# Optimization experiments

Measured on AMD Instinct MI355X. Metric: run time of the kernel, lower is better.

## Reference

```python
import jax, jax.numpy as jnp
import numpy as np

jax.config.update("jax_enable_x64", True)  # original uses complex128 FFTs

H0 = W0 = 3072   # full frame (shp_0)
HC = WC = 2048   # center_dims
MS_H = MS_W = 10
EPS = 1e-8


def setup_inputs() -> dict:
    key = jax.random.key(0)
    k1, k2 = jax.random.split(key)
    # smooth base image so the NCC peak neighborhood is positive (log-valid),
    # as the algorithm assumes for real microscopy data
    base = jax.image.resize(jax.random.normal(k1, (192, 192), jnp.float32), (H0, W0), method="linear")
    fr = jnp.roll(base, (3, -2), axis=(0, 1))[None, :, :, None] + 0.02 * jax.random.normal(k2, (1, H0, W0, 1), jnp.float32)
    template = base[:, :, None, None]
    return {"fr": fr.astype(jnp.float32), "template": template.astype(jnp.float32)}


def _avg_pool_valid(x, kh, kw):
    # x: (1,H,W,C); stride-1 VALID average pool via summed-area table (kernel is huge: ~2028x2028)
    s = jnp.cumsum(jnp.cumsum(x.astype(jnp.float64), axis=1), axis=2)
    s = jnp.pad(s, ((0, 0), (1, 0), (1, 0), (0, 0)))
    H, W = x.shape[1], x.shape[2]
    oh, ow = H - kh + 1, W - kw + 1
    sums = (s[:, kh:kh + oh, kw:kw + ow] - s[:, :oh, kw:kw + ow]
            - s[:, kh:kh + oh, :ow] + s[:, :oh, :ow])
    return (sums / (kh * kw)).astype(x.dtype)


def _extract_fractional_peak(ncc, ms_h, ms_w):
    n = ncc[0, :, :, 0]                     # (2*ms_w+1, 2*ms_h+1)
    W = n.shape[1]
    am = jnp.argmax(n.reshape(-1))
    sx = (am // W).astype(jnp.int32)
    sy = (am % W).astype(jnp.int32)
    log_n = jnp.log(n)
    lxm1 = log_n[sx - 1, sy]
    lxp1 = log_n[sx + 1, sy]
    lym1 = log_n[sx, sy - 1]
    lyp1 = log_n[sx, sy + 1]
    four = 4.0 * log_n[sx, sy]
    sh_x = -(sx - ms_h).astype(jnp.float32) - (lxm1 - lxp1) / (2.0 * lxm1 - four + 2.0 * lxp1)
    sh_y = -(sy - ms_w).astype(jnp.float32) - (lym1 - lyp1) / (2.0 * lym1 - four + 2.0 * lyp1)
    return sh_x.reshape(1, 1), sh_y.reshape(1, 1)


def _translate_bilinear(img, dx, dy):
    # tfa.image.translate semantics: out[r,c] = bilinear img[r - dy, c - dx], zero fill outside
    H, W = img.shape
    r = jnp.arange(H, dtype=img.dtype)[:, None] - dy   # (H,1)
    c = jnp.arange(W, dtype=img.dtype)[None, :] - dx   # (1,W)
    r0 = jnp.floor(r)
    c0 = jnp.floor(c)
    wr = r - r0
    wc = c - c0
    r0i = r0.astype(jnp.int32)
    c0i = c0.astype(jnp.int32)

    def samp(ri, ci):
        valid = (ri >= 0) & (ri < H) & (ci >= 0) & (ci < W)
        v = img[jnp.clip(ri, 0, H - 1), jnp.clip(ci, 0, W - 1)]  # index broadcast -> (H,W)
        return jnp.where(valid, v, jnp.zeros((), img.dtype))

    return (samp(r0i, c0i) * (1 - wr) * (1 - wc)
            + samp(r0i, c0i + 1) * (1 - wr) * wc
            + samp(r0i + 1, c0i) * wr * (1 - wc)
            + samp(r0i + 1, c0i + 1) * wr * wc)


def _forward(fr, template):
    scx = (H0 - HC) // 2
    scy = (W0 - WC) // 2
    tmpl = template[scx:H0 - scx, scy:W0 - scy]             # (HC,WC,1,1)
    shp_prod = float(HC * WC)
    mx, my = HC // 2, WC // 2

    # template normalization (done once in __init__ originally)
    t_zm = tmpl - jnp.mean(tmpl, axis=(0, 1), keepdims=True)
    t_var = jnp.sum(jnp.square(t_zm), axis=(0, 1), keepdims=True) + EPS   # (1,1,1,1)
    target_freq = jnp.fft.fftn(t_zm[:, :, :, 0].astype(jnp.complex128), axes=(0, 1, 2))

    fr_center = fr[0, scx:H0 - scx, scy:W0 - scy][None]     # (1,HC,WC,1)
    imgs_zm = fr_center - jnp.mean(fr_center, axis=(1, 2), keepdims=True)
    img_stack = jnp.stack([fr_center[:, :, :, 0], jnp.square(fr_center)[:, :, :, 0]], axis=3)
    local_mean = _avg_pool_valid(img_stack, HC - 2 * MS_W, WC - 2 * MS_H)  # (1,21,21,2)
    imgs_var = local_mean[..., 1:2] - jnp.square(local_mean[..., 0:1]) / shp_prod + EPS
    imgs_var = jnp.where(imgs_var < 0, jnp.zeros_like(imgs_var), imgs_var)
    denom = jnp.sqrt(t_var * imgs_var)                      # (1,21,21,1)

    fr_freq = jnp.fft.fftn(imgs_zm[0].astype(jnp.complex128), axes=(0, 1, 2))
    cc = jnp.abs(jnp.fft.ifftn(fr_freq * jnp.conj(target_freq), axes=(0, 1, 2))).astype(jnp.float32)[None]
    rolled = jnp.roll(cc, (mx, my), axis=(1, 2))
    ncc = rolled[:, mx - MS_W:mx + MS_W + 1, my - MS_H:my + MS_H + 1] / denom
    ncc = jnp.where(jnp.isnan(ncc), jnp.zeros_like(ncc), ncc)

    sh_x, sh_y = _extract_fractional_peak(ncc, MS_H, MS_W)
    fr_corr = _translate_bilinear(fr[0, :, :, 0], sh_x[0, 0], sh_y[0, 0])
    flat = jnp.reshape(fr_corr.T, (-1,))[None, :]
    return flat, sh_x, sh_y


def reference(fr, template):
    return _forward(fr, template)
```

## Files before the change

kernel.cpp:

```cpp
#include <hip/hip_runtime.h>
#include <math.h>

#define H0 3072
#define HC 2048
#define OFF 512
#define NA 21
#define NAB 441
#define KWIN 2028

#define TB 32
#define YCB 128
#define NTB 64
#define NYB 16
#define NBLK (NTB * NYB)
#define ILDS_STR 136
#define ILDS_ROWS 63
#define ILDS_BYTES (ILDS_ROWS * ILDS_STR * 2)
#define T_ROWE 176
#define T_ROWW 88
#define CSTR_DW 2824
#define CSTR_E  5648
#define TLDS_BYTES (4 * CSTR_DW * 4)

#define WS_SCAL 128
#define WS_P1   256
#define WS_TT   12800
#define WS_RS   13312
#define WS_R    32768
#define WS_R2   376832
#define WS_DEN  720896
#define WS_CCV  724992
#define WS_CP   786432

typedef __attribute__((ext_vector_type(8))) short short8;
typedef __attribute__((ext_vector_type(4))) float f32x4;

static __device__ __forceinline__ unsigned f2bf_pack(float a, float b) {
    union { float f; unsigned u; } x, y; x.f = a; y.f = b;
    unsigned ra = (x.u + 0x7fff + ((x.u >> 16) & 1)) >> 16;
    unsigned rb = (y.u + 0x7fff + ((y.u >> 16) & 1)) >> 16;
    return ra | (rb << 16);
}

__global__ void k_sums(const float* __restrict__ tp, double* __restrict__ p1) {
    __shared__ double rs[8];
    double st = 0, st2 = 0;
    const int n4 = (HC * HC) / 4;
    for (int i = blockIdx.x * blockDim.x + threadIdx.x; i < n4; i += gridDim.x * blockDim.x) {
        int x = i >> 9, y4 = (i & 511) * 4;
        float4 t4 = *(const float4*)&tp[(size_t)(OFF + x) * H0 + OFF + y4];
        st += ((double)t4.x + t4.y) + ((double)t4.z + t4.w);
        st2 += ((double)t4.x * t4.x + (double)t4.y * t4.y) +
               ((double)t4.z * t4.z + (double)t4.w * t4.w);
    }
    int tid = threadIdx.x;
    for (int o = 32; o > 0; o >>= 1) { st += __shfl_down(st, o); st2 += __shfl_down(st2, o); }
    if ((tid & 63) == 0) { rs[tid >> 6] = st; rs[4 + (tid >> 6)] = st2; }
    __syncthreads();
    if (tid == 0) {
        p1[blockIdx.x * 2 + 0] = rs[0] + rs[1] + rs[2] + rs[3];
        p1[blockIdx.x * 2 + 1] = rs[4] + rs[5] + rs[6] + rs[7];
    }
}

__global__ void k_sums_final(const double* __restrict__ p1, const double* __restrict__ rowsum,
                             float* __restrict__ scal) {
    __shared__ double rs[512 * 3];
    int tid = threadIdx.x;
    double sf = rowsum[tid] + rowsum[512 + tid] + rowsum[1024 + tid] + rowsum[1536 + tid];
    rs[tid] = p1[tid * 2 + 0];
    rs[512 + tid] = p1[tid * 2 + 1];
    rs[1024 + tid] = sf;
    __syncthreads();
    for (int off = 256; off > 0; off >>= 1) {
        if (tid < off) {
            rs[tid] += rs[tid + off];
            rs[512 + tid] += rs[512 + tid + off];
            rs[1024 + tid] += rs[1024 + tid + off];
        }
        __syncthreads();
    }
    if (tid == 0) {
        double N = (double)HC * (double)HC;
        double st = rs[0], st2 = rs[512], sfd = rs[1024];
        float mt = (float)(st / N);
        float mf = (float)(sfd / N);
        double m = (double)mt;
        double tv = st2 - 2.0 * m * st + N * m * m;
        scal[0] = mt;
        scal[1] = mf;
        scal[2] = (float)tv + 1e-8f;
    }
}

__global__ void k_rowpool(const float* __restrict__ fr,
                          double* __restrict__ Rv, double* __restrict__ Rv2,
                          double* __restrict__ rowsum) {
    __shared__ float row[2048];
    __shared__ double s1[8], s2[8];
    int x = blockIdx.x, tid = threadIdx.x;
    const float* src = fr + (size_t)(OFF + x) * H0 + OFF;
    float4 v0 = *(const float4*)&src[4 * tid];
    float4 v1 = *(const float4*)&src[4 * tid + 1024];
    *(float4*)&row[4 * tid] = v0;
    *(float4*)&row[4 * tid + 1024] = v1;
    double a = ((double)v0.x + v0.y) + ((double)v0.z + v0.w) +
               ((double)v1.x + v1.y) + ((double)v1.z + v1.w);
    double b = ((double)v0.x * v0.x + (double)v0.y * v0.y) +
               ((double)v0.z * v0.z + (double)v0.w * v0.w) +
               ((double)v1.x * v1.x + (double)v1.y * v1.y) +
               ((double)v1.z * v1.z + (double)v1.w * v1.w);
    for (int o = 32; o > 0; o >>= 1) { a += __shfl_down(a, o); b += __shfl_down(b, o); }
    if ((tid & 63) == 0) { s1[tid >> 6] = a; s2[tid >> 6] = b; }
    __syncthreads();
    if (tid == 0) {
        double A = s1[0] + s1[1] + s1[2] + s1[3];
        double B = s2[0] + s2[1] + s2[2] + s2[3];
        rowsum[x] = A;
        s1[0] = A; s2[0] = B;
    }
    __syncthreads();
    if (tid < NA) {
        double h1 = 0, h2 = 0;
        for (int y = 0; y < tid; y++)          { float v = row[y]; h1 += v; h2 += (double)v * v; }
        for (int y = tid + KWIN; y < 2048; y++){ float v = row[y]; h1 += v; h2 += (double)v * v; }
        Rv [(size_t)tid * 2048 + x] = s1[0] - h1;
        Rv2[(size_t)tid * 2048 + x] = s2[0] - h2;
    }
}

__global__ void k_colsum(const double* __restrict__ Rv, const double* __restrict__ Rv2,
                         double* __restrict__ TT) {
    __shared__ double red[256];
    int b = blockIdx.x, tid = threadIdx.x;
    const double* R = (b >= NA) ? (Rv2 + (size_t)(b - NA) * 2048)
                                : (Rv  + (size_t)b * 2048);
    double s = 0;
    for (int x = tid; x < 2048; x += 256) s += R[x];
    red[tid] = s;
    __syncthreads();
    for (int off = 128; off > 0; off >>= 1) {
        if (tid < off) red[tid] += red[tid + off];
        __syncthreads();
    }
    if (tid == 0) TT[b] = red[0];
}

__global__ void k_den(const double* __restrict__ Rv, const double* __restrict__ Rv2,
                      const double* __restrict__ TT, const float* __restrict__ scal,
                      float* __restrict__ den) {
    int tid = threadIdx.x;
    if (tid >= NAB) return;
    int i = tid / NA, j = tid - (tid / NA) * NA;
    const double* R0 = Rv  + (size_t)j * 2048;
    const double* R1 = Rv2 + (size_t)j * 2048;
    double h0 = 0, h1 = 0;
    for (int x = 0; x < i; x++)           { h0 += R0[x]; h1 += R1[x]; }
    for (int x = i + KWIN; x < 2048; x++) { h0 += R0[x]; h1 += R1[x]; }
    double area = (double)KWIN * (double)KWIN;
    float lm0 = (float)((TT[j] - h0) / area);
    float lm1 = (float)((TT[NA + j] - h1) / area);
    float iv = lm1 - (lm0 * lm0) / 4194304.0f + 1e-8f;
    if (iv < 0.f) iv = 0.f;
    den[tid] = sqrtf(scal[2] * iv);
}

__global__ __launch_bounds__(256) void k_corr(const float* __restrict__ fr,
                                              const float* __restrict__ tp,
                                              const float* __restrict__ scal,
                                              float* __restrict__ cp) {
    __shared__ __align__(16) char smem[ILDS_BYTES + TLDS_BYTES];
    unsigned short* Il = (unsigned short*)smem;
    unsigned short* Tl = (unsigned short*)(smem + ILDS_BYTES);
    unsigned* Iw = (unsigned*)smem;
    unsigned* Tw = (unsigned*)Tl;
    int tid = threadIdx.x;
    int bid = blockIdx.x;
    int t0 = (bid >> 4) * TB;
    int y0 = (bid & 15) * YCB;
    float mt = scal[0], mf = scal[1];

    for (int idx = tid; idx < ILDS_ROWS * 32; idx += 256) {
        int row = idx >> 5, pc4 = idx & 31;
        int grow = (t0 - 10 + row) & (HC - 1);
        float4 v = *(const float4*)&fr[(size_t)(OFF + grow) * H0 + OFF + y0 + 4 * pc4];
        uint2 pk;
        pk.x = f2bf_pack(v.x - mf, v.y - mf);
        pk.y = f2bf_pack(v.z - mf, v.w - mf);
        *(uint2*)(Iw + row * (ILDS_STR / 2) + 2 * pc4) = pk;
    }
    for (int u = tid; u < TB * 11; u += 256) {
        int row = u / 11, k = u - row * 11;
        int e0 = 16 * k;
        const float* srcT = tp + (size_t)(OFF + t0 + row) * H0 + OFF;
        unsigned w[10];
#pragma unroll
        for (int q4 = 0; q4 < 5; ++q4) {
            int gcol = (y0 - 24 + e0 + 4 * q4) & (HC - 1);
            float4 v = *(const float4*)&srcT[gcol];
            w[2 * q4]     = f2bf_pack(v.x - mt, v.y - mt);
            w[2 * q4 + 1] = f2bf_pack(v.z - mt, v.w - mt);
        }
        unsigned* dst = Tw + row * T_ROWW + 8 * k;
        uint4 c0a = {w[0], w[1], w[2], w[3]};
        uint4 c0b = {w[4], w[5], w[6], w[7]};
        *(uint4*)(dst) = c0a;
        *(uint4*)(dst + 4) = c0b;
        unsigned d1[8], d2[8], d3[8];
#pragma unroll
        for (int j = 0; j < 8; ++j) {
            d1[j] = (w[j] >> 16) | (w[j + 1] << 16);
            d2[j] = w[j + 1];
            d3[j] = (w[j + 1] >> 16) | (w[j + 2] << 16);
        }
        uint4 c1a = {d1[0], d1[1], d1[2], d1[3]}, c1b = {d1[4], d1[5], d1[6], d1[7]};
        uint4 c2a = {d2[0], d2[1], d2[2], d2[3]}, c2b = {d2[4], d2[5], d2[6], d2[7]};
        uint4 c3a = {d3[0], d3[1], d3[2], d3[3]}, c3b = {d3[4], d3[5], d3[6], d3[7]};
        *(uint4*)(dst + CSTR_DW) = c1a;     *(uint4*)(dst + CSTR_DW + 4) = c1b;
        *(uint4*)(dst + 2 * CSTR_DW) = c2a; *(uint4*)(dst + 2 * CSTR_DW + 4) = c2b;
        *(uint4*)(dst + 3 * CSTR_DW) = c3a; *(uint4*)(dst + 3 * CSTR_DW + 4) = c3b;
    }
    __syncthreads();

    int l = tid & 63, wv = tid >> 6;
    int kg = l >> 4, i16 = l & 15;
    f32x4 acc00 = {0.f, 0.f, 0.f, 0.f};
    f32x4 acc01 = {0.f, 0.f, 0.f, 0.f};
    f32x4 acc10 = {0.f, 0.f, 0.f, 0.f};
    f32x4 acc11 = {0.f, 0.f, 0.f, 0.f};

    for (int dt = 0; dt < 8; ++dt) {
        int t_loc = 8 * wv + dt;
        const unsigned short* Trow = Tl + t_loc * T_ROWE;
        const unsigned short* Ir0 = Il + (t_loc + i16) * ILDS_STR;
        const unsigned short* Ir1 = Ir0 + 16 * ILDS_STR;
#pragma unroll
        for (int ks = 0; ks < 4; ++ks) {
            int yk = 32 * ks + 8 * kg;
            short8 a0 = *(const short8*)(Ir0 + yk);
            short8 a1 = *(const short8*)(Ir1 + yk);
            union { uint2 u[2]; short8 s; } ub0, ub1;
            {
                int s0 = yk - i16 + 34;
                int c = s0 & 3;
                const unsigned short* q = Trow + c * CSTR_E + (s0 - c);
                ub0.u[0] = *(const uint2*)q;
                ub0.u[1] = *(const uint2*)(q + 4);
            }
            {
                int s0 = yk - i16 + 18;
                int c = s0 & 3;
                const unsigned short* q = Trow + c * CSTR_E + (s0 - c);
                ub1.u[0] = *(const uint2*)q;
                ub1.u[1] = *(const uint2*)(q + 4);
            }
            acc00 = __builtin_amdgcn_mfma_f32_16x16x32_bf16(a0, ub0.s, acc00, 0, 0, 0);
            acc01 = __builtin_amdgcn_mfma_f32_16x16x32_bf16(a0, ub1.s, acc01, 0, 0, 0);
            acc10 = __builtin_amdgcn_mfma_f32_16x16x32_bf16(a1, ub0.s, acc10, 0, 0, 0);
            acc11 = __builtin_amdgcn_mfma_f32_16x16x32_bf16(a1, ub1.s, acc11, 0, 0, 0);
        }
    }

    __syncthreads();
    float* buf = (float*)smem;
    {
        int r0w = 4 * kg;
#pragma unroll
        for (int r = 0; r < 4; ++r) {
            buf[wv * 1024 + (r0w + r) * 32 + i16]           = acc00[r];
            buf[wv * 1024 + (r0w + r) * 32 + 16 + i16]      = acc01[r];
            buf[wv * 1024 + (16 + r0w + r) * 32 + i16]      = acc10[r];
            buf[wv * 1024 + (16 + r0w + r) * 32 + 16 + i16] = acc11[r];
        }
    }
    __syncthreads();
    for (int e = tid; e < 1024; e += 256) {
        int a = e >> 5, b = e & 31;
        if (a < NA && b < NA)
            cp[(size_t)bid * NAB + a * NA + b] =
                buf[e] + buf[1024 + e] + buf[2048 + e] + buf[3072 + e];
    }
}

__global__ void k_ccreduce(const float* __restrict__ cp, double* __restrict__ ccv) {
    __shared__ double red[256];
    int ab = blockIdx.x, tid = threadIdx.x;
    double s = 0;
    for (int blk = tid; blk < NBLK; blk += 256) s += (double)cp[(size_t)blk * NAB + ab];
    red[tid] = s;
    __syncthreads();
    for (int off = 128; off > 0; off >>= 1) {
        if (tid < off) red[tid] += red[tid + off];
        __syncthreads();
    }
    if (tid == 0) ccv[ab] = red[0];
}

__global__ void k_peak(const double* __restrict__ ccv, const float* __restrict__ den,
                       float* __restrict__ scal, float* __restrict__ out) {
    __shared__ float ncc[NAB];
    __shared__ float bv[512];
    __shared__ int bi_[512];
    int tid = threadIdx.x;
    if (tid < NAB) {
        float c = fabsf((float)ccv[tid]);
        float v = c / den[tid];
        if (v != v) v = 0.f;
        ncc[tid] = v;
    }
    __syncthreads();
    bv[tid] = (tid < NAB) ? ncc[tid] : -1e38f;
    bi_[tid] = (tid < NAB) ? tid : 0;
    __syncthreads();
    for (int off = 256; off > 0; off >>= 1) {
        if (tid < off) {
            float v2 = bv[tid + off]; int i2 = bi_[tid + off];
            if (v2 > bv[tid] || (v2 == bv[tid] && i2 < bi_[tid])) { bv[tid] = v2; bi_[tid] = i2; }
        }
        __syncthreads();
    }
    if (tid == 0) {
        int am = bi_[0];
        int sx = am / NA, sy = am - (am / NA) * NA;
        auto L = [&](int i, int j) {
            int ii = ((i % NA) + NA) % NA;
            int jj = ((j % NA) + NA) % NA;
            return logf(ncc[ii * NA + jj]);
        };
        float l0 = L(sx, sy);
        float lxm = L(sx - 1, sy), lxp = L(sx + 1, sy);
        float lym = L(sx, sy - 1), lyp = L(sx, sy + 1);
        float four = 4.f * l0;
        float shx = -(float)(sx - 10) - (lxm - lxp) / (2.f * lxm - four + 2.f * lxp);
        float shy = -(float)(sy - 10) - (lym - lyp) / (2.f * lym - four + 2.f * lyp);
        scal[3] = shx; scal[4] = shy;
        out[(size_t)H0 * H0]     = shx;
        out[(size_t)H0 * H0 + 1] = shy;
    }
}

__global__ __launch_bounds__(256) void k_translate(const float* __restrict__ fr,
                                                   const float* __restrict__ scal,
                                                   float* __restrict__ out) {
    __shared__ float T[65 * 67];
    int tid = threadIdx.x;
    int bx = blockIdx.x % 48, by = blockIdx.x / 48;
    int r0 = bx * 64, c0 = by * 64;
    float dx = scal[3], dy = scal[4];
    float fy = -dy, Fy = floorf(fy), wr = fy - Fy;
    float fx = -dx, Fx = floorf(fx), wc = fx - Fx;
    int R0 = r0 + (int)Fy, C0 = c0 + (int)Fx;
    for (int idx = tid; idx < 65 * 65; idx += 256) {
        int i = idx / 65, j = idx - i * 65;
        int gr = R0 + i, gc = C0 + j;
        float v = 0.f;
        if (gr >= 0 && gr < H0 && gc >= 0 && gc < H0) v = fr[(size_t)gr * H0 + gc];
        T[i * 67 + j] = v;
    }
    __syncthreads();
    float w00 = (1.f - wr) * (1.f - wc), w01 = (1.f - wr) * wc;
    float w10 = wr * (1.f - wc),        w11 = wr * wc;
    int rl = (tid & 15) * 4;
    int cl0 = tid >> 4;
    auto S = [&](int rr, int cl) {
        return w00 * T[rr * 67 + cl] + w01 * T[rr * 67 + cl + 1] +
               w10 * T[(rr + 1) * 67 + cl] + w11 * T[(rr + 1) * 67 + cl + 1];
    };
    for (int q = 0; q < 4; q++) {
        int cl = cl0 + q * 16;
        float4 res = make_float4(S(rl, cl), S(rl + 1, cl), S(rl + 2, cl), S(rl + 3, cl));
        *reinterpret_cast<float4*>(&out[(size_t)(c0 + cl) * H0 + r0 + rl]) = res;
    }
}

extern "C" void kernel_launch(void* const* d_in, const int* in_sizes, int n_in,
                              void* d_out, int out_size, void* d_ws, size_t ws_size,
                              hipStream_t stream) {
    const float* fr = (const float*)d_in[0];
    const float* tp = (const float*)d_in[1];
    float* out = (float*)d_out;
    char* ws = (char*)d_ws;
    float*  scal = (float*)(ws + WS_SCAL);
    double* p1   = (double*)(ws + WS_P1);
    double* TT   = (double*)(ws + WS_TT);
    double* rsum = (double*)(ws + WS_RS);
    double* Rv   = (double*)(ws + WS_R);
    double* Rv2  = (double*)(ws + WS_R2);
    float*  den  = (float*)(ws + WS_DEN);
    double* ccv  = (double*)(ws + WS_CCV);
    float*  cp   = (float*)(ws + WS_CP);

    k_rowpool   <<<2048, 256, 0, stream>>>(fr, Rv, Rv2, rsum);
    k_sums      <<<512, 256, 0, stream>>>(tp, p1);
    k_sums_final<<<1, 512, 0, stream>>>(p1, rsum, scal);
    k_colsum    <<<2 * NA, 256, 0, stream>>>(Rv, Rv2, TT);
    k_den       <<<1, 512, 0, stream>>>(Rv, Rv2, TT, scal, den);
    k_corr      <<<NBLK, 256, 0, stream>>>(fr, tp, scal, cp);
    k_ccreduce  <<<NAB, 256, 0, stream>>>(cp, ccv);
    k_peak      <<<1, 512, 0, stream>>>(ccv, den, scal, out);
    k_translate <<<2304, 256, 0, stream>>>(fr, scal, out);
}
```

Before: 83.66 us.

## Fuse template statistics into rowpool, merge colsum/den, double corr rows per block

Template sum and sum-of-squares are now computed inside the row-pooling kernel, so the separate reduction kernel goes away. The column-sum and denominator kernels merge into one kernel with a block per column offset. The correlation kernel now covers 64 template rows per block in two 32-row stages, with a taller image tile in LDS. Together this removes two launches and halves the correlation blocks and their partial outputs, at the cost of fewer blocks for occupancy and extra syncs inside the correlation loop.

```diff
diff --git a/kernel.cpp b/kernel.cpp
--- a/kernel.cpp
+++ b/kernel.cpp
@@ -8,13 +8,13 @@
 #define NAB 441
 #define KWIN 2028
 
-#define TB 32
+#define TCH 64
 #define YCB 128
-#define NTB 64
+#define NTB 32
 #define NYB 16
 #define NBLK (NTB * NYB)
 #define ILDS_STR 136
-#define ILDS_ROWS 63
+#define ILDS_ROWS 95
 #define ILDS_BYTES (ILDS_ROWS * ILDS_STR * 2)
 #define T_ROWE 176
 #define T_ROWW 88
@@ -23,13 +23,12 @@
 #define TLDS_BYTES (4 * CSTR_DW * 4)
 
 #define WS_SCAL 128
-#define WS_P1   256
-#define WS_TT   12800
-#define WS_RS   13312
-#define WS_R    32768
-#define WS_R2   376832
-#define WS_DEN  720896
-#define WS_CCV  724992
+#define WS_P1   4096
+#define WS_RS   36864
+#define WS_R    65536
+#define WS_R2   409600
+#define WS_DEN  753664
+#define WS_CCV  757760
 #define WS_CP   786432
 
 typedef __attribute__((ext_vector_type(8))) short short8;
@@ -42,66 +41,17 @@
     return ra | (rb << 16);
 }
 
-__global__ void k_sums(const float* __restrict__ tp, double* __restrict__ p1) {
-    __shared__ double rs[8];
-    double st = 0, st2 = 0;
-    const int n4 = (HC * HC) / 4;
-    for (int i = blockIdx.x * blockDim.x + threadIdx.x; i < n4; i += gridDim.x * blockDim.x) {
-        int x = i >> 9, y4 = (i & 511) * 4;
-        float4 t4 = *(const float4*)&tp[(size_t)(OFF + x) * H0 + OFF + y4];
-        st += ((double)t4.x + t4.y) + ((double)t4.z + t4.w);
-        st2 += ((double)t4.x * t4.x + (double)t4.y * t4.y) +
-               ((double)t4.z * t4.z + (double)t4.w * t4.w);
-    }
-    int tid = threadIdx.x;
-    for (int o = 32; o > 0; o >>= 1) { st += __shfl_down(st, o); st2 += __shfl_down(st2, o); }
-    if ((tid & 63) == 0) { rs[tid >> 6] = st; rs[4 + (tid >> 6)] = st2; }
-    __syncthreads();
-    if (tid == 0) {
-        p1[blockIdx.x * 2 + 0] = rs[0] + rs[1] + rs[2] + rs[3];
-        p1[blockIdx.x * 2 + 1] = rs[4] + rs[5] + rs[6] + rs[7];
-    }
-}
-
-__global__ void k_sums_final(const double* __restrict__ p1, const double* __restrict__ rowsum,
-                             float* __restrict__ scal) {
-    __shared__ double rs[512 * 3];
-    int tid = threadIdx.x;
-    double sf = rowsum[tid] + rowsum[512 + tid] + rowsum[1024 + tid] + rowsum[1536 + tid];
-    rs[tid] = p1[tid * 2 + 0];
-    rs[512 + tid] = p1[tid * 2 + 1];
-    rs[1024 + tid] = sf;
-    __syncthreads();
-    for (int off = 256; off > 0; off >>= 1) {
-        if (tid < off) {
-            rs[tid] += rs[tid + off];
-            rs[512 + tid] += rs[512 + tid + off];
-            rs[1024 + tid] += rs[1024 + tid + off];
-        }
-        __syncthreads();
-    }
-    if (tid == 0) {
-        double N = (double)HC * (double)HC;
-        double st = rs[0], st2 = rs[512], sfd = rs[1024];
-        float mt = (float)(st / N);
-        float mf = (float)(sfd / N);
-        double m = (double)mt;
-        double tv = st2 - 2.0 * m * st + N * m * m;
-        scal[0] = mt;
-        scal[1] = mf;
-        scal[2] = (float)tv + 1e-8f;
-    }
-}
-
-__global__ void k_rowpool(const float* __restrict__ fr,
+__global__ __launch_bounds__(256) void k_rowpool(const float* __restrict__ fr,
+                          const float* __restrict__ tp,
                           double* __restrict__ Rv, double* __restrict__ Rv2,
-                          double* __restrict__ rowsum) {
+                          double* __restrict__ rowsum, double* __restrict__ p1) {
     __shared__ float row[2048];
-    __shared__ double s1[8], s2[8];
+    __shared__ double s1[4], s2[4], s3[4], s4[4];
     int x = blockIdx.x, tid = threadIdx.x;
-    const float* src = fr + (size_t)(OFF + x) * H0 + OFF;
-    float4 v0 = *(const float4*)&src[4 * tid];
-    float4 v1 = *(const float4*)&src[4 * tid + 1024];
+    const float* srcF = fr + (size_t)(OFF + x) * H0 + OFF;
+    const float* srcT = tp + (size_t)(OFF + x) * H0 + OFF;
+    float4 v0 = *(const float4*)&srcF[4 * tid];
+    float4 v1 = *(const float4*)&srcF[4 * tid + 1024];
     *(float4*)&row[4 * tid] = v0;
     *(float4*)&row[4 * tid + 1024] = v1;
     double a = ((double)v0.x + v0.y) + ((double)v0.z + v0.w) +
@@ -110,13 +60,29 @@
                ((double)v0.z * v0.z + (double)v0.w * v0.w) +
                ((double)v1.x * v1.x + (double)v1.y * v1.y) +
                ((double)v1.z * v1.z + (double)v1.w * v1.w);
-    for (int o = 32; o > 0; o >>= 1) { a += __shfl_down(a, o); b += __shfl_down(b, o); }
-    if ((tid & 63) == 0) { s1[tid >> 6] = a; s2[tid >> 6] = b; }
+    float4 t0 = *(const float4*)&srcT[4 * tid];
+    float4 t1 = *(const float4*)&srcT[4 * tid + 1024];
+    double st = ((double)t0.x + t0.y) + ((double)t0.z + t0.w) +
+                ((double)t1.x + t1.y) + ((double)t1.z + t1.w);
+    double st2 = ((double)t0.x * t0.x + (double)t0.y * t0.y) +
+                 ((double)t0.z * t0.z + (double)t0.w * t0.w) +
+                 ((double)t1.x * t1.x + (double)t1.y * t1.y) +
+                 ((double)t1.z * t1.z + (double)t1.w * t1.w);
+    for (int o = 32; o > 0; o >>= 1) {
+        a += __shfl_down(a, o); b += __shfl_down(b, o);
+        st += __shfl_down(st, o); st2 += __shfl_down(st2, o);
+    }
+    if ((tid & 63) == 0) {
+        int w = tid >> 6;
+        s1[w] = a; s2[w] = b; s3[w] = st; s4[w] = st2;
+    }
     __syncthreads();
     if (tid == 0) {
         double A = s1[0] + s1[1] + s1[2] + s1[3];
         double B = s2[0] + s2[1] + s2[2] + s2[3];
         rowsum[x] = A;
+        p1[2 * x]     = s3[0] + s3[1] + s3[2] + s3[3];
+        p1[2 * x + 1] = s4[0] + s4[1] + s4[2] + s4[3];
         s1[0] = A; s2[0] = B;
     }
     __syncthreads();
@@ -129,40 +95,63 @@
     }
 }
 
-__global__ void k_colsum(const double* __restrict__ Rv, const double* __restrict__ Rv2,
-                         double* __restrict__ TT) {
-    __shared__ double red[256];
-    int b = blockIdx.x, tid = threadIdx.x;
-    const double* R = (b >= NA) ? (Rv2 + (size_t)(b - NA) * 2048)
-                                : (Rv  + (size_t)b * 2048);
-    double s = 0;
-    for (int x = tid; x < 2048; x += 256) s += R[x];
-    red[tid] = s;
-    __syncthreads();
-    for (int off = 128; off > 0; off >>= 1) {
-        if (tid < off) red[tid] += red[tid + off];
-        __syncthreads();
-    }
-    if (tid == 0) TT[b] = red[0];
-}
-
-__global__ void k_den(const double* __restrict__ Rv, const double* __restrict__ Rv2,
-                      const double* __restrict__ TT, const float* __restrict__ scal,
-                      float* __restrict__ den) {
+__global__ void k_scal(const double* __restrict__ p1, const double* __restrict__ rowsum,
+                       float* __restrict__ scal) {
+    __shared__ double rs[512 * 3];
     int tid = threadIdx.x;
-    if (tid >= NAB) return;
-    int i = tid / NA, j = tid - (tid / NA) * NA;
+    double st = 0, st2 = 0, sf = 0;
+    for (int k = 0; k < 4; k++) {
+        int x = tid + 512 * k;
+        st += p1[2 * x]; st2 += p1[2 * x + 1]; sf += rowsum[x];
+    }
+    rs[tid] = st; rs[512 + tid] = st2; rs[1024 + tid] = sf;
+    __syncthreads();
+    for (int off = 256; off > 0; off >>= 1) {
+        if (tid < off) {
+            rs[tid] += rs[tid + off];
+            rs[512 + tid] += rs[512 + tid + off];
+            rs[1024 + tid] += rs[1024 + tid + off];
+        }
+        __syncthreads();
+    }
+    if (tid == 0) {
+        double N = (double)HC * (double)HC;
+        double s = rs[0], s2 = rs[512], sfd = rs[1024];
+        float mt = (float)(s / N);
+        float mf = (float)(sfd / N);
+        double m = (double)mt;
+        double tv = s2 - 2.0 * m * s + N * m * m;
+        scal[0] = mt;
+        scal[1] = mf;
+        scal[2] = (float)tv + 1e-8f;
+    }
+}
+
+__global__ void k_dencol(const double* __restrict__ Rv, const double* __restrict__ Rv2,
+                         const float* __restrict__ scal, float* __restrict__ den) {
+    __shared__ double sm0[4], sm1[4];
+    int j = blockIdx.x, tid = threadIdx.x;
     const double* R0 = Rv  + (size_t)j * 2048;
     const double* R1 = Rv2 + (size_t)j * 2048;
-    double h0 = 0, h1 = 0;
-    for (int x = 0; x < i; x++)           { h0 += R0[x]; h1 += R1[x]; }
-    for (int x = i + KWIN; x < 2048; x++) { h0 += R0[x]; h1 += R1[x]; }
-    double area = (double)KWIN * (double)KWIN;
-    float lm0 = (float)((TT[j] - h0) / area);
-    float lm1 = (float)((TT[NA + j] - h1) / area);
-    float iv = lm1 - (lm0 * lm0) / 4194304.0f + 1e-8f;
-    if (iv < 0.f) iv = 0.f;
-    den[tid] = sqrtf(scal[2] * iv);
+    double s0 = 0, s1 = 0;
+    for (int x = tid; x < 2048; x += 256) { s0 += R0[x]; s1 += R1[x]; }
+    for (int o = 32; o > 0; o >>= 1) { s0 += __shfl_down(s0, o); s1 += __shfl_down(s1, o); }
+    if ((tid & 63) == 0) { sm0[tid >> 6] = s0; sm1[tid >> 6] = s1; }
+    __syncthreads();
+    if (tid < NA) {
+        double T0 = sm0[0] + sm0[1] + sm0[2] + sm0[3];
+        double T1 = sm1[0] + sm1[1] + sm1[2] + sm1[3];
+        int i = tid;
+        double h0 = 0, h1 = 0;
+        for (int x = 0; x < i; x++)           { h0 += R0[x]; h1 += R1[x]; }
+        for (int x = i + KWIN; x < 2048; x++) { h0 += R0[x]; h1 += R1[x]; }
+        double area = (double)KWIN * (double)KWIN;
+        float lm0 = (float)((T0 - h0) / area);
+        float lm1 = (float)((T1 - h1) / area);
+        float iv = lm1 - (lm0 * lm0) / 4194304.0f + 1e-8f;
+        if (iv < 0.f) iv = 0.f;
+        den[i * NA + j] = sqrtf(scal[2] * iv);
+    }
 }
 
 __global__ __launch_bounds__(256) void k_corr(const float* __restrict__ fr,
@@ -176,7 +165,7 @@
     unsigned* Tw = (unsigned*)Tl;
     int tid = threadIdx.x;
     int bid = blockIdx.x;
-    int t0 = (bid >> 4) * TB;
+    int t0 = (bid >> 4) * TCH;
     int y0 = (bid & 15) * YCB;
     float mt = scal[0], mf = scal[1];
 
@@ -189,38 +178,6 @@
         pk.y = f2bf_pack(v.z - mf, v.w - mf);
         *(uint2*)(Iw + row * (ILDS_STR / 2) + 2 * pc4) = pk;
     }
-    for (int u = tid; u < TB * 11; u += 256) {
-        int row = u / 11, k = u - row * 11;
-        int e0 = 16 * k;
-        const float* srcT = tp + (size_t)(OFF + t0 + row) * H0 + OFF;
-        unsigned w[10];
-#pragma unroll
-        for (int q4 = 0; q4 < 5; ++q4) {
-            int gcol = (y0 - 24 + e0 + 4 * q4) & (HC - 1);
-            float4 v = *(const float4*)&srcT[gcol];
-            w[2 * q4]     = f2bf_pack(v.x - mt, v.y - mt);
-            w[2 * q4 + 1] = f2bf_pack(v.z - mt, v.w - mt);
-        }
-        unsigned* dst = Tw + row * T_ROWW + 8 * k;
-        uint4 c0a = {w[0], w[1], w[2], w[3]};
-        uint4 c0b = {w[4], w[5], w[6], w[7]};
-        *(uint4*)(dst) = c0a;
-        *(uint4*)(dst + 4) = c0b;
-        unsigned d1[8], d2[8], d3[8];
-#pragma unroll
-        for (int j = 0; j < 8; ++j) {
-            d1[j] = (w[j] >> 16) | (w[j + 1] << 16);
-            d2[j] = w[j + 1];
-            d3[j] = (w[j + 1] >> 16) | (w[j + 2] << 16);
-        }
-        uint4 c1a = {d1[0], d1[1], d1[2], d1[3]}, c1b = {d1[4], d1[5], d1[6], d1[7]};
-        uint4 c2a = {d2[0], d2[1], d2[2], d2[3]}, c2b = {d2[4], d2[5], d2[6], d2[7]};
-        uint4 c3a = {d3[0], d3[1], d3[2], d3[3]}, c3b = {d3[4], d3[5], d3[6], d3[7]};
-        *(uint4*)(dst + CSTR_DW) = c1a;     *(uint4*)(dst + CSTR_DW + 4) = c1b;
-        *(uint4*)(dst + 2 * CSTR_DW) = c2a; *(uint4*)(dst + 2 * CSTR_DW + 4) = c2b;
-        *(uint4*)(dst + 3 * CSTR_DW) = c3a; *(uint4*)(dst + 3 * CSTR_DW + 4) = c3b;
-    }
-    __syncthreads();
 
     int l = tid & 63, wv = tid >> 6;
     int kg = l >> 4, i16 = l & 15;
@@ -229,39 +186,74 @@
     f32x4 acc10 = {0.f, 0.f, 0.f, 0.f};
     f32x4 acc11 = {0.f, 0.f, 0.f, 0.f};
 
-    for (int dt = 0; dt < 8; ++dt) {
-        int t_loc = 8 * wv + dt;
-        const unsigned short* Trow = Tl + t_loc * T_ROWE;
-        const unsigned short* Ir0 = Il + (t_loc + i16) * ILDS_STR;
-        const unsigned short* Ir1 = Ir0 + 16 * ILDS_STR;
+    for (int s = 0; s < 2; ++s) {
+        for (int u = tid; u < 32 * 11; u += 256) {
+            int row = u / 11, k = u - row * 11;
+            int e0 = 16 * k;
+            const float* srcT = tp + (size_t)(OFF + t0 + 32 * s + row) * H0 + OFF;
+            unsigned w[10];
 #pragma unroll
-        for (int ks = 0; ks < 4; ++ks) {
-            int yk = 32 * ks + 8 * kg;
-            short8 a0 = *(const short8*)(Ir0 + yk);
-            short8 a1 = *(const short8*)(Ir1 + yk);
-            union { uint2 u[2]; short8 s; } ub0, ub1;
-            {
-                int s0 = yk - i16 + 34;
-                int c = s0 & 3;
-                const unsigned short* q = Trow + c * CSTR_E + (s0 - c);
-                ub0.u[0] = *(const uint2*)q;
-                ub0.u[1] = *(const uint2*)(q + 4);
+            for (int q4 = 0; q4 < 5; ++q4) {
+                int gcol = (y0 - 24 + e0 + 4 * q4) & (HC - 1);
+                float4 v = *(const float4*)&srcT[gcol];
+                w[2 * q4]     = f2bf_pack(v.x - mt, v.y - mt);
+                w[2 * q4 + 1] = f2bf_pack(v.z - mt, v.w - mt);
             }
-            {
-                int s0 = yk - i16 + 18;
-                int c = s0 & 3;
-                const unsigned short* q = Trow + c * CSTR_E + (s0 - c);
-                ub1.u[0] = *(const uint2*)q;
-                ub1.u[1] = *(const uint2*)(q + 4);
+            unsigned* dst = Tw + row * T_ROWW + 8 * k;
+            uint4 c0a = {w[0], w[1], w[2], w[3]};
+            uint4 c0b = {w[4], w[5], w[6], w[7]};
+            *(uint4*)(dst) = c0a;
+            *(uint4*)(dst + 4) = c0b;
+            unsigned d1[8], d2[8], d3[8];
+#pragma unroll
+            for (int jj = 0; jj < 8; ++jj) {
+                d1[jj] = (w[jj] >> 16) | (w[jj + 1] << 16);
+                d2[jj] = w[jj + 1];
+                d3[jj] = (w[jj + 1] >> 16) | (w[jj + 2] << 16);
             }
-            acc00 = __builtin_amdgcn_mfma_f32_16x16x32_bf16(a0, ub0.s, acc00, 0, 0, 0);
-            acc01 = __builtin_amdgcn_mfma_f32_16x16x32_bf16(a0, ub1.s, acc01, 0, 0, 0);
-            acc10 = __builtin_amdgcn_mfma_f32_16x16x32_bf16(a1, ub0.s, acc10, 0, 0, 0);
-            acc11 = __builtin_amdgcn_mfma_f32_16x16x32_bf16(a1, ub1.s, acc11, 0, 0, 0);
-        }
-    }
-
-    __syncthreads();
+            uint4 c1a = {d1[0], d1[1], d1[2], d1[3]}, c1b = {d1[4], d1[5], d1[6], d1[7]};
+            uint4 c2a = {d2[0], d2[1], d2[2], d2[3]}, c2b = {d2[4], d2[5], d2[6], d2[7]};
+            uint4 c3a = {d3[0], d3[1], d3[2], d3[3]}, c3b = {d3[4], d3[5], d3[6], d3[7]};
+            *(uint4*)(dst + CSTR_DW) = c1a;     *(uint4*)(dst + CSTR_DW + 4) = c1b;
+            *(uint4*)(dst + 2 * CSTR_DW) = c2a; *(uint4*)(dst + 2 * CSTR_DW + 4) = c2b;
+            *(uint4*)(dst + 3 * CSTR_DW) = c3a; *(uint4*)(dst + 3 * CSTR_DW + 4) = c3b;
+        }
+        __syncthreads();
+
+        for (int dt = 0; dt < 8; ++dt) {
+            int tl = 8 * wv + dt;
+            const unsigned short* Trow = Tl + tl * T_ROWE;
+            const unsigned short* Ir0 = Il + (32 * s + tl + i16) * ILDS_STR;
+            const unsigned short* Ir1 = Ir0 + 16 * ILDS_STR;
+#pragma unroll
+            for (int ks = 0; ks < 4; ++ks) {
+                int yk = 32 * ks + 8 * kg;
+                short8 a0 = *(const short8*)(Ir0 + yk);
+                short8 a1 = *(const short8*)(Ir1 + yk);
+                union { uint2 u[2]; short8 s; } ub0, ub1;
+                {
+                    int s0 = yk - i16 + 34;
+                    int c = s0 & 3;
+                    const unsigned short* q = Trow + c * CSTR_E + (s0 - c);
+                    ub0.u[0] = *(const uint2*)q;
+                    ub0.u[1] = *(const uint2*)(q + 4);
+                }
+                {
+                    int s0 = yk - i16 + 18;
+                    int c = s0 & 3;
+                    const unsigned short* q = Trow + c * CSTR_E + (s0 - c);
+                    ub1.u[0] = *(const uint2*)q;
+                    ub1.u[1] = *(const uint2*)(q + 4);
+                }
+                acc00 = __builtin_amdgcn_mfma_f32_16x16x32_bf16(a0, ub0.s, acc00, 0, 0, 0);
+                acc01 = __builtin_amdgcn_mfma_f32_16x16x32_bf16(a0, ub1.s, acc01, 0, 0, 0);
+                acc10 = __builtin_amdgcn_mfma_f32_16x16x32_bf16(a1, ub0.s, acc10, 0, 0, 0);
+                acc11 = __builtin_amdgcn_mfma_f32_16x16x32_bf16(a1, ub1.s, acc11, 0, 0, 0);
+            }
+        }
+        __syncthreads();
+    }
+
     float* buf = (float*)smem;
     {
         int r0w = 4 * kg;
@@ -382,7 +374,6 @@
     char* ws = (char*)d_ws;
     float*  scal = (float*)(ws + WS_SCAL);
     double* p1   = (double*)(ws + WS_P1);
-    double* TT   = (double*)(ws + WS_TT);
     double* rsum = (double*)(ws + WS_RS);
     double* Rv   = (double*)(ws + WS_R);
     double* Rv2  = (double*)(ws + WS_R2);
@@ -390,11 +381,9 @@
     double* ccv  = (double*)(ws + WS_CCV);
     float*  cp   = (float*)(ws + WS_CP);
 
-    k_rowpool   <<<2048, 256, 0, stream>>>(fr, Rv, Rv2, rsum);
-    k_sums      <<<512, 256, 0, stream>>>(tp, p1);
-    k_sums_final<<<1, 512, 0, stream>>>(p1, rsum, scal);
-    k_colsum    <<<2 * NA, 256, 0, stream>>>(Rv, Rv2, TT);
-    k_den       <<<1, 512, 0, stream>>>(Rv, Rv2, TT, scal, den);
+    k_rowpool   <<<2048, 256, 0, stream>>>(fr, tp, Rv, Rv2, rsum, p1);
+    k_scal      <<<1, 512, 0, stream>>>(p1, rsum, scal);
+    k_dencol    <<<NA, 256, 0, stream>>>(Rv, Rv2, scal, den);
     k_corr      <<<NBLK, 256, 0, stream>>>(fr, tp, scal, cp);
     k_ccreduce  <<<NAB, 256, 0, stream>>>(cp, ccv);
     k_peak      <<<1, 512, 0, stream>>>(ccv, den, scal, out);
```

Measured after the change: 71.16 us. -14.9%, faster.
